# Kernel optimization log

Hardware: AMD Instinct MI355X
Metric: run time of the kernel (lower is better)

Reference implementation:

```python
import jax, jax.numpy as jnp
import numpy as np

N_NODES = 100000
N_EDGES = 1600000
D = 64
N_LAYERS = 5
N_GRAPHS = 256


def setup_inputs() -> dict:
    key = jax.random.key(0)
    ks = jax.random.split(key, 12)
    x = jax.random.normal(ks[0], (N_NODES, D), dtype=jnp.float32)
    edge_index = jax.random.randint(ks[1], (2, N_EDGES), 0, N_NODES, dtype=jnp.int64)
    batch = jnp.sort(jax.random.randint(ks[2], (N_NODES,), 0, N_GRAPHS, dtype=jnp.int64))
    s = 1.0 / np.sqrt(D)
    # stacked GINConv MLP params: Linear(D,D) -> ReLU -> Linear(D,D), per layer
    Ws1 = jax.random.uniform(ks[3], (N_LAYERS, D, D), jnp.float32, -s, s)
    bs1 = jax.random.uniform(ks[4], (N_LAYERS, D), jnp.float32, -s, s)
    Ws2 = jax.random.uniform(ks[5], (N_LAYERS, D, D), jnp.float32, -s, s)
    bs2 = jax.random.uniform(ks[6], (N_LAYERS, D), jnp.float32, -s, s)
    # final readout MLP: Linear(D,D) -> ReLU -> Linear(D,D)
    mW1 = jax.random.uniform(ks[7], (D, D), jnp.float32, -s, s)
    mb1 = jax.random.uniform(ks[8], (D,), jnp.float32, -s, s)
    mW2 = jax.random.uniform(ks[9], (D, D), jnp.float32, -s, s)
    mb2 = jax.random.uniform(ks[10], (D,), jnp.float32, -s, s)
    return {"x": x, "edge_index": edge_index, "batch": batch,
            "Ws1": Ws1, "bs1": bs1, "Ws2": Ws2, "bs2": bs2,
            "mW1": mW1, "mb1": mb1, "mW2": mW2, "mb2": mb2}


def reference(x, edge_index, batch, Ws1, bs1, Ws2, bs2, mW1, mb1, mW2, mb2):
    src, dst = edge_index[0], edge_index[1]
    h = x
    for l in range(N_LAYERS):
        # GINConv (eps=0): MLP(h + sum_{j in N(i)} h_j)
        agg = jax.ops.segment_sum(h[src], dst, num_segments=N_NODES)
        z = h + agg
        z = jax.nn.relu(z @ Ws1[l] + bs1[l])
        h = z @ Ws2[l] + bs2[l]
    # global mean pool over graphs
    sums = jax.ops.segment_sum(h, batch, num_segments=N_GRAPHS)
    cnts = jax.ops.segment_sum(jnp.ones((h.shape[0],), h.dtype), batch, num_segments=N_GRAPHS)
    pooled = sums / jnp.maximum(cnts, 1.0)[:, None]
    # readout MLP
    out = jax.nn.relu(pooled @ mW1 + mb1) @ mW2 + mb2
    return out
```

## Files before the change

### kernel.cpp

```cpp
#include <hip/hip_runtime.h>
#include <hip/hip_bf16.h>

#define N_NODES 100000
#define N_EDGES 1600000
#define DIM 64
#define N_LAYERS 5
#define N_GRAPHS 256

#define NB2 196
#define SUBCAP2 9216
#define CAP2 12800
#define DUMMY N_NODES
#define TILE 3200
#define NTILE 500
#define MTILES (N_NODES / 16)

typedef __attribute__((ext_vector_type(8))) short short8;
typedef __attribute__((ext_vector_type(4))) float float4v;

__global__ void zero_kernel(int* p, int n) {
    int i = blockIdx.x * blockDim.x + threadIdx.x;
    if (i < n) p[i] = 0;
}

__device__ __forceinline__ unsigned short f2bf(float f) {
    unsigned int u = __float_as_uint(f);
    unsigned int r = (u + 0x7fffu + ((u >> 16) & 1u)) >> 16;
    return (unsigned short)r;
}
__device__ __forceinline__ float bf2f(unsigned short b) {
    return __uint_as_float(((unsigned int)b) << 16);
}

__global__ void zero_dummy_kernel(unsigned short* a, unsigned short* b) {
    int t = threadIdx.x;
    a[(size_t)DUMMY * DIM + t] = 0;
    b[(size_t)DUMMY * DIM + t] = 0;
}

__global__ void cvt_kernel(const float4* __restrict__ x, ushort4* __restrict__ hb, int n4) {
    int i = blockIdx.x * blockDim.x + threadIdx.x;
    if (i < n4) {
        float4 v = x[i];
        ushort4 o;
        o.x = f2bf(v.x); o.y = f2bf(v.y); o.z = f2bf(v.z); o.w = f2bf(v.w);
        hb[i] = o;
    }
}

__global__ void prepack_kernel(const float* __restrict__ Ws1, const float* __restrict__ Ws2,
                               unsigned short* __restrict__ wpk) {
    int t = blockIdx.x * blockDim.x + threadIdx.x;
    if (t >= N_LAYERS * 32 * 64) return;
    int lane = t & 63;
    int frag = (t >> 6) & 31;
    int l = t >> 11;
    int kf = frag & 1;
    int nt = (frag >> 1) & 3;
    int split = (frag >> 3) & 1;
    int mat = (frag >> 4) & 1;
    const float* W = (mat ? Ws2 : Ws1) + (size_t)l * DIM * DIM;
    unsigned short outv[8];
#pragma unroll
    for (int j = 0; j < 8; ++j) {
        int k = kf * 32 + ((lane >> 4) << 3) + j;
        int n = nt * 16 + (lane & 15);
        float v = W[k * DIM + n];
        unsigned short hi = f2bf(v);
        outv[j] = split ? f2bf(v - bf2f(hi)) : hi;
    }
    ushort4* dst = (ushort4*)(wpk + ((size_t)(l * 32 + frag) * 64 + lane) * 8);
    dst[0] = make_ushort4(outv[0], outv[1], outv[2], outv[3]);
    dst[1] = make_ushort4(outv[4], outv[5], outv[6], outv[7]);
}

__global__ __launch_bounds__(256) void bin_kernel(
    const int* __restrict__ src, const int* __restrict__ dst,
    int* __restrict__ bcursor, int* __restrict__ pairbuf) {
    __shared__ int hcnt[NB2];
    __shared__ int gbase[NB2];
    __shared__ int lcur[NB2];
    const int tid = threadIdx.x;
    const int base = blockIdx.x * TILE;

    for (int l = tid; l < NB2; l += 256) { hcnt[l] = 0; lcur[l] = 0; }
    __syncthreads();
    for (int j = tid; j < TILE; j += 256) {
        int d = dst[base + j];
        atomicAdd(&hcnt[d >> 9], 1);
    }
    __syncthreads();
    for (int l = tid; l < NB2; l += 256)
        gbase[l] = atomicAdd(&bcursor[l], hcnt[l]);
    __syncthreads();
    for (int j = tid; j < TILE; j += 256) {
        int s = src[base + j];
        int d = dst[base + j];
        int b = d >> 9;
        int r = atomicAdd(&lcur[b], 1);
        int pos = gbase[b] + r;
        if (pos < SUBCAP2) pairbuf[b * SUBCAP2 + pos] = (s << 9) | (d & 511);
    }
}

__global__ __launch_bounds__(256) void csr_kernel(
    const int* __restrict__ bcursor, const int* __restrict__ pairbuf,
    int* __restrict__ esrc, int2* __restrict__ meta) {
    __shared__ int lcnt[512];
    __shared__ int loff[512];
    __shared__ int lcur[512];
    __shared__ int s2[256];
    const int b = blockIdx.x;
    const int tid = threadIdx.x;
    int ec = bcursor[b];
    if (ec > SUBCAP2) ec = SUBCAP2;
    const int* pp = pairbuf + b * SUBCAP2;

    for (int l = tid; l < 512; l += 256) lcnt[l] = 0;
    __syncthreads();
    for (int j = tid; j < ec; j += 256) atomicAdd(&lcnt[pp[j] & 511], 1);
    __syncthreads();

    int c0 = (lcnt[2 * tid] + 7) & ~7;
    int c1 = (lcnt[2 * tid + 1] + 7) & ~7;
    s2[tid] = c0 + c1;
    __syncthreads();
    for (int off = 1; off < 256; off <<= 1) {
        int v = (tid >= off) ? s2[tid - off] : 0;
        __syncthreads();
        s2[tid] += v;
        __syncthreads();
    }
    int exc = s2[tid] - (c0 + c1);
    loff[2 * tid] = exc;
    loff[2 * tid + 1] = exc + c0;
    __syncthreads();

    int* eb = esrc + (size_t)b * CAP2;
    for (int l = tid; l < 512; l += 256) {
        int st = loff[l];
        int cn = lcnt[l];
        int cp = (cn + 7) & ~7;
        lcur[l] = st;
        int node = b * 512 + l;
        if (node < N_NODES) meta[node] = make_int2(b * CAP2 + st, cp);
        for (int j = cn; j < cp; ++j) eb[st + j] = DUMMY;
    }
    __syncthreads();

    for (int j = tid; j < ec; j += 256) {
        int p = pp[j];
        int pos = atomicAdd(&lcur[p & 511], 1);
        eb[pos] = p >> 9;
    }
}

__device__ __forceinline__ void acc8(float* acc, uint4 v) {
    acc[0] += __uint_as_float(v.x << 16);
    acc[1] += __uint_as_float(v.x & 0xffff0000u);
    acc[2] += __uint_as_float(v.y << 16);
    acc[3] += __uint_as_float(v.y & 0xffff0000u);
    acc[4] += __uint_as_float(v.z << 16);
    acc[5] += __uint_as_float(v.z & 0xffff0000u);
    acc[6] += __uint_as_float(v.w << 16);
    acc[7] += __uint_as_float(v.w & 0xffff0000u);
}

__global__ __launch_bounds__(256) void agg_kernel(
    const unsigned short* __restrict__ hin, unsigned short* __restrict__ z,
    const int2* __restrict__ meta, const int* __restrict__ esrc, int n_nodes) {
    __shared__ float zbuf[4][2][8][DIM];
    const int lane = threadIdx.x & 63;
    const int wv = threadIdx.x >> 6;
    const int grp = lane >> 3;
    const int sub = lane & 7;
    const int wave_id = (blockIdx.x * blockDim.x + threadIdx.x) >> 6;
    const int n_waves = (gridDim.x * blockDim.x) >> 6;
    const uint4* __restrict__ h4 = (const uint4*)hin;

    for (int ii = wave_id; 2 * ii < n_nodes; ii += n_waves) {
        const int iA = 2 * ii;
        const int iB = iA + 1;
        const int2 mA = meta[iA];
        const int2 mB = meta[iB];
        const float selfA = bf2f(hin[iA * DIM + lane]);
        const float selfB = bf2f(hin[iB * DIM + lane]);
        const int* eA = esrc + mA.x + grp;
        const int* eB = esrc + mB.x + grp;
        const int nA = mA.y, nB = mB.y;

        float accA[8], accB[8];
#pragma unroll
        for (int j = 0; j < 8; ++j) { accA[j] = 0.f; accB[j] = 0.f; }

        int k = 0;
        const int nmin = (nA < nB) ? nA : nB;
        for (; k < nmin; k += 8) {
            const int ia = eA[k];
            const int ib = eB[k];
            uint4 va = h4[ia * 8 + sub];
            uint4 vb = h4[ib * 8 + sub];
            acc8(accA, va);
            acc8(accB, vb);
        }
        for (int kk = k; kk < nA; kk += 8) {
            uint4 va = h4[eA[kk] * 8 + sub];
            acc8(accA, va);
        }
        for (int kk = k; kk < nB; kk += 8) {
            uint4 vb = h4[eB[kk] * 8 + sub];
            acc8(accB, vb);
        }

        *((float4*)&zbuf[wv][0][grp][sub * 8 + 0]) = make_float4(accA[0], accA[1], accA[2], accA[3]);
        *((float4*)&zbuf[wv][0][grp][sub * 8 + 4]) = make_float4(accA[4], accA[5], accA[6], accA[7]);
        *((float4*)&zbuf[wv][1][grp][sub * 8 + 0]) = make_float4(accB[0], accB[1], accB[2], accB[3]);
        *((float4*)&zbuf[wv][1][grp][sub * 8 + 4]) = make_float4(accB[4], accB[5], accB[6], accB[7]);
        __builtin_amdgcn_wave_barrier();
        float zA = selfA, zB = selfB;
#pragma unroll
        for (int g = 0; g < 8; ++g) {
            zA += zbuf[wv][0][g][lane];
            zB += zbuf[wv][1][g][lane];
        }
        z[iA * DIM + lane] = f2bf(zA);
        z[iB * DIM + lane] = f2bf(zB);
        __builtin_amdgcn_wave_barrier();
    }
}

__device__ __forceinline__ short8 load_frag(const unsigned short* __restrict__ wl, int frag, int lane) {
    union { uint4 u; short8 s; } c;
    c.u = *(const uint4*)(wl + ((size_t)(frag * 64 + lane)) * 8);
    return c.s;
}

__device__ __forceinline__ void split8(const float* v, short8& hi, short8& lo) {
#pragma unroll
    for (int j = 0; j < 8; ++j) {
        unsigned short h = f2bf(v[j]);
        hi[j] = (short)h;
        lo[j] = (short)f2bf(v[j] - bf2f(h));
    }
}

__global__ __launch_bounds__(256) void mlp_mfma_kernel(
    const unsigned short* __restrict__ z, unsigned short* __restrict__ hout,
    const unsigned short* __restrict__ wl,
    const float* __restrict__ b1, const float* __restrict__ b2) {
    __shared__ float tbuf[4][16][68];
    const int lane = threadIdx.x & 63;
    const int wv = threadIdx.x >> 6;
    const int m = lane & 15;
    const int quad = lane >> 4;
    const int wave_id = (blockIdx.x * blockDim.x + threadIdx.x) >> 6;
    const int n_waves = (gridDim.x * blockDim.x) >> 6;

    float b1v[4], b2v[4];
#pragma unroll
    for (int nt = 0; nt < 4; ++nt) {
        b1v[nt] = b1[nt * 16 + m];
        b2v[nt] = b2[nt * 16 + m];
    }

    for (int tile = wave_id; tile < MTILES; tile += n_waves) {
        const int node0 = tile * 16;

        short8 a1[2];
#pragma unroll
        for (int kf = 0; kf < 2; ++kf) {
            union { uint4 u; short8 s; } c;
            c.u = *(const uint4*)(z + ((size_t)(node0 + m)) * DIM + kf * 32 + quad * 8);
            a1[kf] = c.s;
        }

        float4v acc1[4] = {};
#pragma unroll
        for (int nt = 0; nt < 4; ++nt) {
#pragma unroll
            for (int kf = 0; kf < 2; ++kf) {
                short8 bhi = load_frag(wl, ((0 * 2 + 0) * 4 + nt) * 2 + kf, lane);
                short8 blo = load_frag(wl, ((0 * 2 + 1) * 4 + nt) * 2 + kf, lane);
                acc1[nt] = __builtin_amdgcn_mfma_f32_16x16x32_bf16(a1[kf], bhi, acc1[nt], 0, 0, 0);
                acc1[nt] = __builtin_amdgcn_mfma_f32_16x16x32_bf16(a1[kf], blo, acc1[nt], 0, 0, 0);
            }
        }

#pragma unroll
        for (int nt = 0; nt < 4; ++nt) {
#pragma unroll
            for (int r = 0; r < 4; ++r) {
                float tv = acc1[nt][r] + b1v[nt];
                tbuf[wv][quad * 4 + r][nt * 16 + m] = fmaxf(tv, 0.f);
            }
        }
        __builtin_amdgcn_wave_barrier();

        short8 a2hi[2], a2lo[2];
#pragma unroll
        for (int kf = 0; kf < 2; ++kf) {
            const float4* tp = (const float4*)&tbuf[wv][m][kf * 32 + quad * 8];
            float4 t0 = tp[0];
            float4 t1 = tp[1];
            float v[8] = {t0.x, t0.y, t0.z, t0.w, t1.x, t1.y, t1.z, t1.w};
            split8(v, a2hi[kf], a2lo[kf]);
        }
        __builtin_amdgcn_wave_barrier();

        float4v acc2[4] = {};
#pragma unroll
        for (int nt = 0; nt < 4; ++nt) {
#pragma unroll
            for (int kf = 0; kf < 2; ++kf) {
                short8 bhi = load_frag(wl, ((1 * 2 + 0) * 4 + nt) * 2 + kf, lane);
                short8 blo = load_frag(wl, ((1 * 2 + 1) * 4 + nt) * 2 + kf, lane);
                acc2[nt] = __builtin_amdgcn_mfma_f32_16x16x32_bf16(a2hi[kf], bhi, acc2[nt], 0, 0, 0);
                acc2[nt] = __builtin_amdgcn_mfma_f32_16x16x32_bf16(a2hi[kf], blo, acc2[nt], 0, 0, 0);
                acc2[nt] = __builtin_amdgcn_mfma_f32_16x16x32_bf16(a2lo[kf], bhi, acc2[nt], 0, 0, 0);
            }
        }

#pragma unroll
        for (int nt = 0; nt < 4; ++nt) {
#pragma unroll
            for (int r = 0; r < 4; ++r) {
                float o = acc2[nt][r] + b2v[nt];
                hout[((size_t)(node0 + quad * 4 + r)) * DIM + nt * 16 + m] = f2bf(o);
            }
        }
    }
}

__global__ __launch_bounds__(256) void pool_mlp_kernel(
    const unsigned short* __restrict__ h, const int* __restrict__ batch,
    const float* __restrict__ mW1, const float* __restrict__ mb1,
    const float* __restrict__ mW2, const float* __restrict__ mb2,
    float* __restrict__ out, int n_nodes) {
    __shared__ float part[4][DIM];
    const int g = blockIdx.x;
    const int lane = threadIdx.x & 63;
    const int w = threadIdx.x >> 6;

    int lo = 0, hi = n_nodes;
    while (lo < hi) {
        int mid = (lo + hi) >> 1;
        if (batch[mid] < g) lo = mid + 1; else hi = mid;
    }
    const int s0 = lo;
    hi = n_nodes;
    while (lo < hi) {
        int mid = (lo + hi) >> 1;
        if (batch[mid] < g + 1) lo = mid + 1; else hi = mid;
    }
    const int e0 = lo;

    float acc = 0.f;
    int i = s0 + w;
    for (; i + 12 < e0; i += 16) {
        float v0 = bf2f(h[i * DIM + lane]);
        float v1 = bf2f(h[(i + 4) * DIM + lane]);
        float v2 = bf2f(h[(i + 8) * DIM + lane]);
        float v3 = bf2f(h[(i + 12) * DIM + lane]);
        acc += (v0 + v1) + (v2 + v3);
    }
    for (; i < e0; i += 4) acc += bf2f(h[i * DIM + lane]);
    part[w][lane] = acc;
    __syncthreads();

    if (w == 0) {
        acc = (part[0][lane] + part[1][lane]) + (part[2][lane] + part[3][lane]);
        float cntf = (float)(e0 - s0);
        acc /= fmaxf(cntf, 1.f);

        float t = mb1[lane];
#pragma unroll
        for (int d = 0; d < DIM; ++d) {
            float zd = __shfl(acc, d);
            t = fmaf(zd, mW1[d * DIM + lane], t);
        }
        t = fmaxf(t, 0.f);
        float o = mb2[lane];
#pragma unroll
        for (int d = 0; d < DIM; ++d) {
            float rd = __shfl(t, d);
            o = fmaf(rd, mW2[d * DIM + lane], o);
        }
        out[g * DIM + lane] = o;
    }
}

extern "C" void kernel_launch(void* const* d_in, const int* in_sizes, int n_in,
                              void* d_out, int out_size, void* d_ws, size_t ws_size,
                              hipStream_t stream) {
    const float* x   = (const float*)d_in[0];
    const int*   ei  = (const int*)d_in[1];
    const int*   bat = (const int*)d_in[2];
    const float* Ws1 = (const float*)d_in[3];
    const float* bs1 = (const float*)d_in[4];
    const float* Ws2 = (const float*)d_in[5];
    const float* bs2 = (const float*)d_in[6];
    const float* mW1 = (const float*)d_in[7];
    const float* mb1 = (const float*)d_in[8];
    const float* mW2 = (const float*)d_in[9];
    const float* mb2 = (const float*)d_in[10];
    float* out = (float*)d_out;

    char* ws = (char*)d_ws;
    size_t off = 0;
    auto alloc = [&](size_t bytes) {
        void* p = ws + off;
        off += (bytes + 255) & ~(size_t)255;
        return p;
    };
    int*  esrc    = (int*)alloc((size_t)NB2 * CAP2 * 4);
    int2* meta    = (int2*)alloc((size_t)N_NODES * 8);
    unsigned short* hbfA = (unsigned short*)alloc(((size_t)N_NODES + 1) * DIM * 2);
    unsigned short* hbfB = (unsigned short*)alloc(((size_t)N_NODES + 1) * DIM * 2);
    int*  bcursor = (int*)alloc((size_t)NB2 * 4);
    unsigned short* wpk = (unsigned short*)alloc((size_t)N_LAYERS * 32 * 64 * 8 * 2);
    int*   pairbuf = (int*)alloc((size_t)NB2 * SUBCAP2 * 4);
    unsigned short* zbig = (unsigned short*)alloc((size_t)N_NODES * DIM * 2);

    const int* src = ei;
    const int* dst = ei + N_EDGES;

    zero_kernel<<<1, 256, 0, stream>>>(bcursor, NB2);
    bin_kernel<<<NTILE, 256, 0, stream>>>(src, dst, bcursor, pairbuf);
    csr_kernel<<<NB2, 256, 0, stream>>>(bcursor, pairbuf, esrc, meta);

    prepack_kernel<<<(N_LAYERS * 32 * 64 + 255) / 256, 256, 0, stream>>>(Ws1, Ws2, wpk);
    zero_dummy_kernel<<<1, 64, 0, stream>>>(hbfA, hbfB);
    cvt_kernel<<<(N_NODES * DIM / 4 + 255) / 256, 256, 0, stream>>>(
        (const float4*)x, (ushort4*)hbfA, N_NODES * DIM / 4);

    const unsigned short* hin = hbfA;
    unsigned short* hout = hbfB;
    for (int l = 0; l < N_LAYERS; ++l) {
        agg_kernel<<<2048, 256, 0, stream>>>(hin, zbig, meta, esrc, N_NODES);
        mlp_mfma_kernel<<<1024, 256, 0, stream>>>(zbig, hout,
                                                  wpk + (size_t)l * 32 * 64 * 8,
                                                  bs1 + (size_t)l * DIM,
                                                  bs2 + (size_t)l * DIM);
        hin = hout;
        hout = (hout == hbfA) ? hbfB : hbfA;
    }
    pool_mlp_kernel<<<N_GRAPHS, 256, 0, stream>>>(hin, bat, mW1, mb1, mW2, mb2, out, N_NODES);
}
```

Before: 372.9 us.

## Fuse neighbor aggregation and GIN MLP into one per-layer kernel

Merges the aggregation kernel and the MFMA MLP kernel into a single per-layer kernel. Each block aggregates a 16-node tile into swizzled LDS, then four waves each compute one 16-column slice of both linear layers. This removes the global z round trip and one launch per layer. In exchange it adds block-level syncthreads between phases, and load imbalance in the gather phase can stall the MFMA phase.

```diff
diff --git a/kernel.cpp b/kernel.cpp
--- a/kernel.cpp
+++ b/kernel.cpp
@@ -166,167 +166,146 @@
     acc[7] += __uint_as_float(v.w & 0xffff0000u);
 }
 
-__global__ __launch_bounds__(256) void agg_kernel(
-    const unsigned short* __restrict__ hin, unsigned short* __restrict__ z,
-    const int2* __restrict__ meta, const int* __restrict__ esrc, int n_nodes) {
-    __shared__ float zbuf[4][2][8][DIM];
+__device__ __forceinline__ short8 load_frag(const unsigned short* __restrict__ wl, int frag, int lane) {
+    union { uint4 u; short8 s; } c;
+    c.u = *(const uint4*)(wl + ((size_t)(frag * 64 + lane)) * 8);
+    return c.s;
+}
+
+__device__ __forceinline__ void split8(const float* v, short8& hi, short8& lo) {
+#pragma unroll
+    for (int j = 0; j < 8; ++j) {
+        unsigned short h = f2bf(v[j]);
+        hi[j] = (short)h;
+        lo[j] = (short)f2bf(v[j] - bf2f(h));
+    }
+}
+
+__global__ __launch_bounds__(256) void fused_layer_kernel(
+    const unsigned short* __restrict__ hin, unsigned short* __restrict__ hout,
+    const int2* __restrict__ meta, const int* __restrict__ esrc,
+    const unsigned short* __restrict__ wl,
+    const float* __restrict__ b1, const float* __restrict__ b2) {
+    __shared__ float zred[4][2][8][DIM];
+    __shared__ unsigned short zt[16 * DIM];
+    __shared__ float tbuf[16][68];
     const int lane = threadIdx.x & 63;
     const int wv = threadIdx.x >> 6;
     const int grp = lane >> 3;
     const int sub = lane & 7;
-    const int wave_id = (blockIdx.x * blockDim.x + threadIdx.x) >> 6;
-    const int n_waves = (gridDim.x * blockDim.x) >> 6;
-    const uint4* __restrict__ h4 = (const uint4*)hin;
-
-    for (int ii = wave_id; 2 * ii < n_nodes; ii += n_waves) {
-        const int iA = 2 * ii;
-        const int iB = iA + 1;
-        const int2 mA = meta[iA];
-        const int2 mB = meta[iB];
-        const float selfA = bf2f(hin[iA * DIM + lane]);
-        const float selfB = bf2f(hin[iB * DIM + lane]);
-        const int* eA = esrc + mA.x + grp;
-        const int* eB = esrc + mB.x + grp;
-        const int nA = mA.y, nB = mB.y;
-
-        float accA[8], accB[8];
-#pragma unroll
-        for (int j = 0; j < 8; ++j) { accA[j] = 0.f; accB[j] = 0.f; }
-
-        int k = 0;
-        const int nmin = (nA < nB) ? nA : nB;
-        for (; k < nmin; k += 8) {
-            const int ia = eA[k];
-            const int ib = eB[k];
-            uint4 va = h4[ia * 8 + sub];
-            uint4 vb = h4[ib * 8 + sub];
-            acc8(accA, va);
-            acc8(accB, vb);
-        }
-        for (int kk = k; kk < nA; kk += 8) {
-            uint4 va = h4[eA[kk] * 8 + sub];
-            acc8(accA, va);
-        }
-        for (int kk = k; kk < nB; kk += 8) {
-            uint4 vb = h4[eB[kk] * 8 + sub];
-            acc8(accB, vb);
-        }
-
-        *((float4*)&zbuf[wv][0][grp][sub * 8 + 0]) = make_float4(accA[0], accA[1], accA[2], accA[3]);
-        *((float4*)&zbuf[wv][0][grp][sub * 8 + 4]) = make_float4(accA[4], accA[5], accA[6], accA[7]);
-        *((float4*)&zbuf[wv][1][grp][sub * 8 + 0]) = make_float4(accB[0], accB[1], accB[2], accB[3]);
-        *((float4*)&zbuf[wv][1][grp][sub * 8 + 4]) = make_float4(accB[4], accB[5], accB[6], accB[7]);
-        __builtin_amdgcn_wave_barrier();
-        float zA = selfA, zB = selfB;
-#pragma unroll
-        for (int g = 0; g < 8; ++g) {
-            zA += zbuf[wv][0][g][lane];
-            zB += zbuf[wv][1][g][lane];
-        }
-        z[iA * DIM + lane] = f2bf(zA);
-        z[iB * DIM + lane] = f2bf(zB);
-        __builtin_amdgcn_wave_barrier();
-    }
-}
-
-__device__ __forceinline__ short8 load_frag(const unsigned short* __restrict__ wl, int frag, int lane) {
-    union { uint4 u; short8 s; } c;
-    c.u = *(const uint4*)(wl + ((size_t)(frag * 64 + lane)) * 8);
-    return c.s;
-}
-
-__device__ __forceinline__ void split8(const float* v, short8& hi, short8& lo) {
-#pragma unroll
-    for (int j = 0; j < 8; ++j) {
-        unsigned short h = f2bf(v[j]);
-        hi[j] = (short)h;
-        lo[j] = (short)f2bf(v[j] - bf2f(h));
-    }
-}
-
-__global__ __launch_bounds__(256) void mlp_mfma_kernel(
-    const unsigned short* __restrict__ z, unsigned short* __restrict__ hout,
-    const unsigned short* __restrict__ wl,
-    const float* __restrict__ b1, const float* __restrict__ b2) {
-    __shared__ float tbuf[4][16][68];
-    const int lane = threadIdx.x & 63;
-    const int wv = threadIdx.x >> 6;
     const int m = lane & 15;
     const int quad = lane >> 4;
-    const int wave_id = (blockIdx.x * blockDim.x + threadIdx.x) >> 6;
-    const int n_waves = (gridDim.x * blockDim.x) >> 6;
-
-    float b1v[4], b2v[4];
-#pragma unroll
-    for (int nt = 0; nt < 4; ++nt) {
-        b1v[nt] = b1[nt * 16 + m];
-        b2v[nt] = b2[nt * 16 + m];
-    }
-
-    for (int tile = wave_id; tile < MTILES; tile += n_waves) {
+    const int nt = wv;
+    const uint4* __restrict__ h4 = (const uint4*)hin;
+
+    const float b1v = b1[nt * 16 + m];
+    const float b2v = b2[nt * 16 + m];
+
+    for (int tile = blockIdx.x; tile < MTILES; tile += gridDim.x) {
         const int node0 = tile * 16;
 
+#pragma unroll
+        for (int p = 0; p < 2; ++p) {
+            const int iA = node0 + wv * 4 + p * 2;
+            const int iB = iA + 1;
+            const int2 mA = meta[iA];
+            const int2 mB = meta[iB];
+            const float selfA = bf2f(hin[(size_t)iA * DIM + lane]);
+            const float selfB = bf2f(hin[(size_t)iB * DIM + lane]);
+            const int* eA = esrc + mA.x + grp;
+            const int* eB = esrc + mB.x + grp;
+            const int nA = mA.y, nB = mB.y;
+
+            float accA[8], accB[8];
+#pragma unroll
+            for (int j = 0; j < 8; ++j) { accA[j] = 0.f; accB[j] = 0.f; }
+
+            int k = 0;
+            const int nmin = (nA < nB) ? nA : nB;
+            for (; k < nmin; k += 8) {
+                const int ia = eA[k];
+                const int ib = eB[k];
+                uint4 va = h4[ia * 8 + sub];
+                uint4 vb = h4[ib * 8 + sub];
+                acc8(accA, va);
+                acc8(accB, vb);
+            }
+            for (int kk = k; kk < nA; kk += 8) {
+                uint4 va = h4[eA[kk] * 8 + sub];
+                acc8(accA, va);
+            }
+            for (int kk = k; kk < nB; kk += 8) {
+                uint4 vb = h4[eB[kk] * 8 + sub];
+                acc8(accB, vb);
+            }
+
+            *((float4*)&zred[wv][0][grp][sub * 8 + 0]) = make_float4(accA[0], accA[1], accA[2], accA[3]);
+            *((float4*)&zred[wv][0][grp][sub * 8 + 4]) = make_float4(accA[4], accA[5], accA[6], accA[7]);
+            *((float4*)&zred[wv][1][grp][sub * 8 + 0]) = make_float4(accB[0], accB[1], accB[2], accB[3]);
+            *((float4*)&zred[wv][1][grp][sub * 8 + 4]) = make_float4(accB[4], accB[5], accB[6], accB[7]);
+            __builtin_amdgcn_wave_barrier();
+            float zA = selfA, zB = selfB;
+#pragma unroll
+            for (int g = 0; g < 8; ++g) {
+                zA += zred[wv][0][g][lane];
+                zB += zred[wv][1][g][lane];
+            }
+            const int rA = wv * 4 + p * 2;
+            const int rB = rA + 1;
+            zt[rA * DIM + (lane ^ ((rA & 7) << 3))] = f2bf(zA);
+            zt[rB * DIM + (lane ^ ((rB & 7) << 3))] = f2bf(zB);
+            __builtin_amdgcn_wave_barrier();
+        }
+        __syncthreads();
+
         short8 a1[2];
 #pragma unroll
         for (int kf = 0; kf < 2; ++kf) {
-            union { uint4 u; short8 s; } c;
-            c.u = *(const uint4*)(z + ((size_t)(node0 + m)) * DIM + kf * 32 + quad * 8);
-            a1[kf] = c.s;
-        }
-
-        float4v acc1[4] = {};
-#pragma unroll
-        for (int nt = 0; nt < 4; ++nt) {
-#pragma unroll
-            for (int kf = 0; kf < 2; ++kf) {
-                short8 bhi = load_frag(wl, ((0 * 2 + 0) * 4 + nt) * 2 + kf, lane);
-                short8 blo = load_frag(wl, ((0 * 2 + 1) * 4 + nt) * 2 + kf, lane);
-                acc1[nt] = __builtin_amdgcn_mfma_f32_16x16x32_bf16(a1[kf], bhi, acc1[nt], 0, 0, 0);
-                acc1[nt] = __builtin_amdgcn_mfma_f32_16x16x32_bf16(a1[kf], blo, acc1[nt], 0, 0, 0);
-            }
-        }
-
-#pragma unroll
-        for (int nt = 0; nt < 4; ++nt) {
-#pragma unroll
-            for (int r = 0; r < 4; ++r) {
-                float tv = acc1[nt][r] + b1v[nt];
-                tbuf[wv][quad * 4 + r][nt * 16 + m] = fmaxf(tv, 0.f);
-            }
-        }
-        __builtin_amdgcn_wave_barrier();
+            const int c = (kf * 32 + quad * 8) ^ ((m & 7) << 3);
+            union { uint4 u; short8 s; } cu;
+            cu.u = *(const uint4*)(zt + m * DIM + c);
+            a1[kf] = cu.s;
+        }
+        short8 w1hi0 = load_frag(wl, 0 * 16 + 0 * 8 + nt * 2 + 0, lane);
+        short8 w1lo0 = load_frag(wl, 0 * 16 + 1 * 8 + nt * 2 + 0, lane);
+        short8 w1hi1 = load_frag(wl, 0 * 16 + 0 * 8 + nt * 2 + 1, lane);
+        short8 w1lo1 = load_frag(wl, 0 * 16 + 1 * 8 + nt * 2 + 1, lane);
+        float4v acc1 = {};
+        acc1 = __builtin_amdgcn_mfma_f32_16x16x32_bf16(a1[0], w1hi0, acc1, 0, 0, 0);
+        acc1 = __builtin_amdgcn_mfma_f32_16x16x32_bf16(a1[0], w1lo0, acc1, 0, 0, 0);
+        acc1 = __builtin_amdgcn_mfma_f32_16x16x32_bf16(a1[1], w1hi1, acc1, 0, 0, 0);
+        acc1 = __builtin_amdgcn_mfma_f32_16x16x32_bf16(a1[1], w1lo1, acc1, 0, 0, 0);
+
+#pragma unroll
+        for (int r = 0; r < 4; ++r)
+            tbuf[quad * 4 + r][nt * 16 + m] = fmaxf(acc1[r] + b1v, 0.f);
+        __syncthreads();
 
         short8 a2hi[2], a2lo[2];
 #pragma unroll
         for (int kf = 0; kf < 2; ++kf) {
-            const float4* tp = (const float4*)&tbuf[wv][m][kf * 32 + quad * 8];
+            const float4* tp = (const float4*)&tbuf[m][kf * 32 + quad * 8];
             float4 t0 = tp[0];
             float4 t1 = tp[1];
             float v[8] = {t0.x, t0.y, t0.z, t0.w, t1.x, t1.y, t1.z, t1.w};
             split8(v, a2hi[kf], a2lo[kf]);
         }
-        __builtin_amdgcn_wave_barrier();
-
-        float4v acc2[4] = {};
-#pragma unroll
-        for (int nt = 0; nt < 4; ++nt) {
-#pragma unroll
-            for (int kf = 0; kf < 2; ++kf) {
-                short8 bhi = load_frag(wl, ((1 * 2 + 0) * 4 + nt) * 2 + kf, lane);
-                short8 blo = load_frag(wl, ((1 * 2 + 1) * 4 + nt) * 2 + kf, lane);
-                acc2[nt] = __builtin_amdgcn_mfma_f32_16x16x32_bf16(a2hi[kf], bhi, acc2[nt], 0, 0, 0);
-                acc2[nt] = __builtin_amdgcn_mfma_f32_16x16x32_bf16(a2hi[kf], blo, acc2[nt], 0, 0, 0);
-                acc2[nt] = __builtin_amdgcn_mfma_f32_16x16x32_bf16(a2lo[kf], bhi, acc2[nt], 0, 0, 0);
-            }
-        }
-
-#pragma unroll
-        for (int nt = 0; nt < 4; ++nt) {
-#pragma unroll
-            for (int r = 0; r < 4; ++r) {
-                float o = acc2[nt][r] + b2v[nt];
-                hout[((size_t)(node0 + quad * 4 + r)) * DIM + nt * 16 + m] = f2bf(o);
-            }
+        short8 w2hi0 = load_frag(wl, 1 * 16 + 0 * 8 + nt * 2 + 0, lane);
+        short8 w2lo0 = load_frag(wl, 1 * 16 + 1 * 8 + nt * 2 + 0, lane);
+        short8 w2hi1 = load_frag(wl, 1 * 16 + 0 * 8 + nt * 2 + 1, lane);
+        short8 w2lo1 = load_frag(wl, 1 * 16 + 1 * 8 + nt * 2 + 1, lane);
+        float4v acc2 = {};
+        acc2 = __builtin_amdgcn_mfma_f32_16x16x32_bf16(a2hi[0], w2hi0, acc2, 0, 0, 0);
+        acc2 = __builtin_amdgcn_mfma_f32_16x16x32_bf16(a2hi[0], w2lo0, acc2, 0, 0, 0);
+        acc2 = __builtin_amdgcn_mfma_f32_16x16x32_bf16(a2lo[0], w2hi0, acc2, 0, 0, 0);
+        acc2 = __builtin_amdgcn_mfma_f32_16x16x32_bf16(a2hi[1], w2hi1, acc2, 0, 0, 0);
+        acc2 = __builtin_amdgcn_mfma_f32_16x16x32_bf16(a2hi[1], w2lo1, acc2, 0, 0, 0);
+        acc2 = __builtin_amdgcn_mfma_f32_16x16x32_bf16(a2lo[1], w2hi1, acc2, 0, 0, 0);
+
+#pragma unroll
+        for (int r = 0; r < 4; ++r) {
+            float o = acc2[r] + b2v;
+            hout[((size_t)(node0 + quad * 4 + r)) * DIM + nt * 16 + m] = f2bf(o);
         }
     }
 }
@@ -419,7 +398,6 @@
     int*  bcursor = (int*)alloc((size_t)NB2 * 4);
     unsigned short* wpk = (unsigned short*)alloc((size_t)N_LAYERS * 32 * 64 * 8 * 2);
     int*   pairbuf = (int*)alloc((size_t)NB2 * SUBCAP2 * 4);
-    unsigned short* zbig = (unsigned short*)alloc((size_t)N_NODES * DIM * 2);
 
     const int* src = ei;
     const int* dst = ei + N_EDGES;
@@ -436,11 +414,10 @@
     const unsigned short* hin = hbfA;
     unsigned short* hout = hbfB;
     for (int l = 0; l < N_LAYERS; ++l) {
-        agg_kernel<<<2048, 256, 0, stream>>>(hin, zbig, meta, esrc, N_NODES);
-        mlp_mfma_kernel<<<1024, 256, 0, stream>>>(zbig, hout,
-                                                  wpk + (size_t)l * 32 * 64 * 8,
-                                                  bs1 + (size_t)l * DIM,
-                                                  bs2 + (size_t)l * DIM);
+        fused_layer_kernel<<<3125, 256, 0, stream>>>(hin, hout, meta, esrc,
+                                                     wpk + (size_t)l * 32 * 64 * 8,
+                                                     bs1 + (size_t)l * DIM,
+                                                     bs2 + (size_t)l * DIM);
         hin = hout;
         hout = (hout == hbfA) ? hbfB : hbfA;
     }
```

After: 424.8 us. 1.14x slower.

## Pipeline neighbor gathers via global_load_lds double-buffered ring in aggregation

Applied to the files above, without the earlier changes.

Replaces the direct register gather of neighbor feature rows with asynchronous global-to-LDS loads (global_load_lds) into a per-wave double-buffered ring. The next batch of edge indices is prefetched while the current ring slot is accumulated, and short neighbor lists are padded with a dummy node index. The intent is to overlap gather latency with accumulation and keep more loads in flight per wave. This depends on hand-written waitcnt counts and on the dummy row at index N_NODES existing and being zero. A mistake in either would corrupt results.

```diff
diff --git a/kernel.cpp b/kernel.cpp
--- a/kernel.cpp
+++ b/kernel.cpp
@@ -166,65 +166,100 @@
     acc[7] += __uint_as_float(v.w & 0xffff0000u);
 }
 
+typedef const __attribute__((address_space(1))) void* as1cv;
+typedef __attribute__((address_space(3))) void* as3v;
+__device__ __forceinline__ void gload16(const void* g, void* l) {
+    __builtin_amdgcn_global_load_lds((as1cv)g, (as3v)l, 16, 0, 0);
+}
+
 __global__ __launch_bounds__(256) void agg_kernel(
     const unsigned short* __restrict__ hin, unsigned short* __restrict__ z,
     const int2* __restrict__ meta, const int* __restrict__ esrc, int n_nodes) {
-    __shared__ float zbuf[4][2][8][DIM];
+    __shared__ char scratch[4][4096];
     const int lane = threadIdx.x & 63;
     const int wv = threadIdx.x >> 6;
     const int grp = lane >> 3;
     const int sub = lane & 7;
     const int wave_id = (blockIdx.x * blockDim.x + threadIdx.x) >> 6;
     const int n_waves = (gridDim.x * blockDim.x) >> 6;
-    const uint4* __restrict__ h4 = (const uint4*)hin;
+    char* ring = scratch[wv];
+    const char* hb = (const char*)hin;
 
     for (int ii = wave_id; 2 * ii < n_nodes; ii += n_waves) {
         const int iA = 2 * ii;
         const int iB = iA + 1;
         const int2 mA = meta[iA];
         const int2 mB = meta[iB];
-        const float selfA = bf2f(hin[iA * DIM + lane]);
-        const float selfB = bf2f(hin[iB * DIM + lane]);
+        const float selfA = bf2f(hin[(size_t)iA * DIM + lane]);
+        const float selfB = bf2f(hin[(size_t)iB * DIM + lane]);
+        const int nA = mA.y, nB = mB.y;
         const int* eA = esrc + mA.x + grp;
         const int* eB = esrc + mB.x + grp;
-        const int nA = mA.y, nB = mB.y;
-
-        float accA[8], accB[8];
-#pragma unroll
-        for (int j = 0; j < 8; ++j) { accA[j] = 0.f; accB[j] = 0.f; }
-
-        int k = 0;
-        const int nmin = (nA < nB) ? nA : nB;
-        for (; k < nmin; k += 8) {
-            const int ia = eA[k];
-            const int ib = eB[k];
-            uint4 va = h4[ia * 8 + sub];
-            uint4 vb = h4[ib * 8 + sub];
-            acc8(accA, va);
-            acc8(accB, vb);
-        }
-        for (int kk = k; kk < nA; kk += 8) {
-            uint4 va = h4[eA[kk] * 8 + sub];
-            acc8(accA, va);
-        }
-        for (int kk = k; kk < nB; kk += 8) {
-            uint4 vb = h4[eB[kk] * 8 + sub];
-            acc8(accB, vb);
-        }
-
-        *((float4*)&zbuf[wv][0][grp][sub * 8 + 0]) = make_float4(accA[0], accA[1], accA[2], accA[3]);
-        *((float4*)&zbuf[wv][0][grp][sub * 8 + 4]) = make_float4(accA[4], accA[5], accA[6], accA[7]);
-        *((float4*)&zbuf[wv][1][grp][sub * 8 + 0]) = make_float4(accB[0], accB[1], accB[2], accB[3]);
-        *((float4*)&zbuf[wv][1][grp][sub * 8 + 4]) = make_float4(accB[4], accB[5], accB[6], accB[7]);
+        const int nb = ((nA > nB) ? nA : nB) >> 3;
+
+        float accA[8] = {0.f, 0.f, 0.f, 0.f, 0.f, 0.f, 0.f, 0.f};
+        float accB[8] = {0.f, 0.f, 0.f, 0.f, 0.f, 0.f, 0.f, 0.f};
+
+        if (nb > 0) {
+            int o;
+            o = (0 < nA) ? 0 : 0;
+            int ia0 = eA[o]; ia0 = (0 < nA) ? ia0 : DUMMY;
+            int ib0 = eB[o]; ib0 = (0 < nB) ? ib0 : DUMMY;
+            o = (8 < nA) ? 8 : 0;
+            int ia1 = eA[o]; ia1 = (8 < nA) ? ia1 : DUMMY;
+            o = (8 < nB) ? 8 : 0;
+            int ib1 = eB[o]; ib1 = (8 < nB) ? ib1 : DUMMY;
+            asm volatile("s_waitcnt lgkmcnt(0)" ::: "memory");
+            gload16(hb + ((size_t)(unsigned)ia0 << 7) + (sub << 4), ring);
+            gload16(hb + ((size_t)(unsigned)ib0 << 7) + (sub << 4), ring + 2048);
+            if (nb > 1) {
+                gload16(hb + ((size_t)(unsigned)ia1 << 7) + (sub << 4), ring + 1024);
+                gload16(hb + ((size_t)(unsigned)ib1 << 7) + (sub << 4), ring + 3072);
+            }
+            asm volatile("" ::: "memory");
+            int t8 = 16;
+            int oA = (t8 < nA) ? t8 : 0;
+            int oB = (t8 < nB) ? t8 : 0;
+            int nxA = eA[oA]; nxA = (t8 < nA) ? nxA : DUMMY;
+            int nxB = eB[oB]; nxB = (t8 < nB) ? nxB : DUMMY;
+
+            for (int b = 0; b < nb; ++b) {
+                if (b + 1 < nb) asm volatile("s_waitcnt vmcnt(4)" ::: "memory");
+                else            asm volatile("s_waitcnt vmcnt(2)" ::: "memory");
+                const int s = (b & 1) << 10;
+                uint4 va = *(const uint4*)(ring + s + lane * 16);
+                uint4 vb = *(const uint4*)(ring + 2048 + s + lane * 16);
+                acc8(accA, va);
+                acc8(accB, vb);
+                if (b + 2 < nb) {
+                    asm volatile("s_waitcnt lgkmcnt(0)" ::: "memory");
+                    gload16(hb + ((size_t)(unsigned)nxA << 7) + (sub << 4), ring + s);
+                    gload16(hb + ((size_t)(unsigned)nxB << 7) + (sub << 4), ring + 2048 + s);
+                    asm volatile("" ::: "memory");
+                    t8 = 8 * (b + 3);
+                    oA = (t8 < nA) ? t8 : 0;
+                    oB = (t8 < nB) ? t8 : 0;
+                    nxA = eA[oA]; nxA = (t8 < nA) ? nxA : DUMMY;
+                    nxB = eB[oB]; nxB = (t8 < nB) ? nxB : DUMMY;
+                }
+            }
+        }
+
+        float* zbA = (float*)ring;
+        float* zbB = (float*)(ring + 2048);
+        *((float4*)&zbA[grp * 64 + sub * 8 + 0]) = make_float4(accA[0], accA[1], accA[2], accA[3]);
+        *((float4*)&zbA[grp * 64 + sub * 8 + 4]) = make_float4(accA[4], accA[5], accA[6], accA[7]);
+        *((float4*)&zbB[grp * 64 + sub * 8 + 0]) = make_float4(accB[0], accB[1], accB[2], accB[3]);
+        *((float4*)&zbB[grp * 64 + sub * 8 + 4]) = make_float4(accB[4], accB[5], accB[6], accB[7]);
         __builtin_amdgcn_wave_barrier();
         float zA = selfA, zB = selfB;
 #pragma unroll
         for (int g = 0; g < 8; ++g) {
-            zA += zbuf[wv][0][g][lane];
-            zB += zbuf[wv][1][g][lane];
-        }
-        z[iA * DIM + lane] = f2bf(zA);
-        z[iB * DIM + lane] = f2bf(zB);
+            zA += zbA[g * 64 + lane];
+            zB += zbB[g * 64 + lane];
+        }
+        z[(size_t)iA * DIM + lane] = f2bf(zA);
+        z[(size_t)iB * DIM + lane] = f2bf(zB);
         __builtin_amdgcn_wave_barrier();
     }
 }
```

Result: no change. 372.0 us (-0.2%).
